# Performance work log

Hardware: AMD Instinct MI355X
Metric: run time of the kernel (lower is better)

Reference implementation:

```python
import jax, jax.numpy as jnp
import numpy as np

H, C = 3, 64  # heads, per-head channels
NEG_SLOPE = 0.2

def setup_inputs() -> dict:
    key = jax.random.key(0)
    ks = jax.random.split(key, 8)
    B, N, D, E = 2, 50000, 128, 800000
    h = jax.random.normal(ks[0], (B, N, D), dtype=jnp.float32)
    edge_index = jax.random.randint(ks[1], (2, E), 0, N, dtype=jnp.int64)
    s = 1.0 / np.sqrt(D)
    W = jax.random.normal(ks[2], (D, H * C), dtype=jnp.float32) * s
    a_src = jax.random.normal(ks[3], (H, C), dtype=jnp.float32) * (1.0 / np.sqrt(C))
    a_dst = jax.random.normal(ks[4], (H, C), dtype=jnp.float32) * (1.0 / np.sqrt(C))
    bias = jnp.zeros((H * C,), dtype=jnp.float32)
    Wo = jax.random.normal(ks[5], (H * C, 1), dtype=jnp.float32) * (1.0 / np.sqrt(H * C))
    bo = jnp.zeros((1,), dtype=jnp.float32)
    return {"h": h, "edge_index": edge_index, "W": W, "a_src": a_src,
            "a_dst": a_dst, "bias": bias, "Wo": Wo, "bo": bo}

def _gat_single(h_b, src, dst, N, W, a_src, a_dst, bias):
    # h_b: [N, D] -> x: [N, H, C]
    x = (h_b @ W).reshape(-1, H, C)
    alpha_s = jnp.einsum('nhc,hc->nh', x, a_src)  # [N, H]
    alpha_d = jnp.einsum('nhc,hc->nh', x, a_dst)  # [N, H]
    e = alpha_s[src] + alpha_d[dst]               # [E', H]
    e = jnp.where(e > 0, e, NEG_SLOPE * e)        # leaky_relu(0.2)
    # segment softmax over edges grouped by destination node
    emax = jax.ops.segment_max(e, dst, num_segments=N)          # [N, H]
    p = jnp.exp(e - emax[dst])
    denom = jax.ops.segment_sum(p, dst, num_segments=N)         # [N, H]
    att = p / (denom[dst] + 1e-16)                               # [E', H]
    out = jax.ops.segment_sum(att[:, :, None] * x[src], dst, num_segments=N)  # [N,H,C]
    return out.reshape(-1, H * C) + bias

def reference(h, edge_index, W, a_src, a_dst, bias, Wo, bo):
    B, N, D = h.shape
    # PyG GATConv default: add self loops
    loops = jnp.arange(N, dtype=edge_index.dtype)
    src = jnp.concatenate([edge_index[0], loops])
    dst = jnp.concatenate([edge_index[1], loops])
    gat = jax.vmap(lambda hb: _gat_single(hb, src, dst, N, W, a_src, a_dst, bias))(h)
    gat = jax.nn.elu(gat)            # [B, N, H*C]; dropout inactive (eval)
    logits = gat @ Wo + bo           # [B, N, 1]
    return logits
```

## Files before the change

kernel.cpp:

```cpp
#include <hip/hip_runtime.h>
#include <hip/hip_bf16.h>
#include <math.h>

typedef __hip_bfloat16 bf16;
typedef __attribute__((ext_vector_type(8))) short short8;
typedef __attribute__((ext_vector_type(4))) short short4v;
typedef __attribute__((ext_vector_type(4))) float f32x4;
typedef __attribute__((ext_vector_type(2))) float f32x2;

#define HC 192
#define DIN 128
#define NEG_SLOPE 0.2f
#define GN 8
#define CAP 56
#define GROWS 128

static inline int cdiv(int a, int b){ return (a + b - 1) / b; }

__device__ inline short f2bf(float f){
  __hip_bfloat16 b = __float2bfloat16(f);
  return __builtin_bit_cast(short, b);
}
__device__ inline float loadf(const void* p, size_t i, int fm){
  return fm ? __bfloat162float(((const bf16*)p)[i]) : ((const float*)p)[i];
}
__device__ inline int eload(const void* p, long long i, int em){
  return em ? (int)(((const long long*)p)[i]) : ((const int*)p)[i];
}

__device__ inline int detect_fm(const unsigned* __restrict__ hw){
  unsigned w = hw[threadIdx.x & 63];
  unsigned expo = (w >> 7) & 0xFF;
  unsigned long long m = __ballot(expo >= 100 && expo <= 135);
  return __popcll(m) > 32;
}
__device__ inline int detect_em(const unsigned* __restrict__ ew){
  unsigned long long m = __ballot(ew[2*(threadIdx.x & 63) + 1] != 0);
  return __popcll(m) < 32;
}

__global__ void k_zero(int* __restrict__ counts, int N){
  int idx = blockIdx.x * 256 + threadIdx.x;
  for (int i = idx; i < N; i += 96 * 256) counts[i] = 0;
}

__global__ __launch_bounds__(512) void k_fused(const void* __restrict__ h,
    const void* __restrict__ W, const void* __restrict__ a_src,
    const void* __restrict__ a_dst, bf16* __restrict__ x,
    float* __restrict__ asp, float* __restrict__ adp,
    const void* __restrict__ ei, int* __restrict__ counts,
    unsigned* __restrict__ srcs, int M, int N, int E, int NBG){
  __shared__ alignas(16) short ldsW[HC * 136];
  __shared__ alignas(16) float asfL[HC];
  __shared__ alignas(16) float adfL[HC];

  if ((int)blockIdx.x >= NBG){
    int em = detect_em((const unsigned*)ei);
    int idx = ((int)blockIdx.x - NBG) * 512 + (int)threadIdx.x;
    if (idx >= E + N) return;
    int s, d;
    if (idx < E){
      s = eload(ei, idx, em);
      d = eload(ei, (long long)E + idx, em);
    } else { s = d = idx - E; }
    if ((unsigned)d >= (unsigned)N) return;
    if ((unsigned)s >= (unsigned)N) s = 0;
    int slot = atomicAdd(&counts[d], 1);
    if (slot >= CAP) return;
    srcs[(size_t)d * CAP + slot] = (unsigned)s;
    return;
  }

  int fm   = detect_fm((const unsigned*)h);
  int tid  = threadIdx.x;
  int w    = tid >> 6;
  int lane = tid & 63;
  int r16  = lane & 15;
  int quad = lane >> 4;
  if (tid < HC)           asfL[tid]        = loadf(a_src, tid, fm);
  else if (tid < 2 * HC)  adfL[tid - HC]   = loadf(a_dst, tid - HC, fm);
  for (int pi = tid; pi < HC * 16; pi += 512){
    int j = pi % HC, dblk = pi / HC;
    short8 v8;
    #pragma unroll
    for (int kk = 0; kk < 8; kk++)
      v8[kk] = f2bf(loadf(W, (size_t)(dblk * 8 + kk) * HC + j, fm));
    *(short8*)&ldsW[j * 136 + dblk * 8] = v8;
  }
  __syncthreads();

  int row  = (int)blockIdx.x * GROWS + w * 16 + r16;
  int lrow = min(row, M - 1);
  f32x4 acc[12];
  #pragma unroll
  for (int i = 0; i < 12; i++) acc[i] = (f32x4){0.f,0.f,0.f,0.f};
  size_t hbase = (size_t)lrow * DIN + quad * 8;
  #pragma unroll
  for (int kb = 0; kb < 4; kb++){
    short8 bh;
    if (fm == 0){
      const float* hf = (const float*)h + hbase + kb * 32;
      float4 a = *(const float4*)hf;
      float4 b = *(const float4*)(hf + 4);
      bh[0]=f2bf(a.x); bh[1]=f2bf(a.y); bh[2]=f2bf(a.z); bh[3]=f2bf(a.w);
      bh[4]=f2bf(b.x); bh[5]=f2bf(b.y); bh[6]=f2bf(b.z); bh[7]=f2bf(b.w);
    } else {
      bh = *(const short8*)((const bf16*)h + hbase + kb * 32);
    }
    #pragma unroll
    for (int nt = 0; nt < 12; nt++){
      short8 aw = *(const short8*)&ldsW[(nt*16 + r16) * 136 + kb * 32 + quad * 8];
      acc[nt] = __builtin_amdgcn_mfma_f32_16x16x32_bf16(aw, bh, acc[nt], 0,0,0);
    }
  }
  if (row < M){
    int bb    = row >= N;
    int nodeR = row - bb * N;
    bf16* xr  = x + ((size_t)nodeR * 2 + bb) * HC;
    #pragma unroll
    for (int nt = 0; nt < 12; nt++){
      short4v pk = { f2bf(acc[nt][0]), f2bf(acc[nt][1]),
                     f2bf(acc[nt][2]), f2bf(acc[nt][3]) };
      *(short4v*)(xr + nt*16 + quad*4) = pk;
    }
  }
  float vs[3] = {0.f,0.f,0.f}, vd[3] = {0.f,0.f,0.f};
  #pragma unroll
  for (int nt = 0; nt < 12; nt++){
    int hh = nt >> 2;
    f32x4 a4 = *(const f32x4*)&asfL[nt*16 + quad*4];
    f32x4 d4 = *(const f32x4*)&adfL[nt*16 + quad*4];
    vs[hh] += acc[nt][0]*a4[0] + acc[nt][1]*a4[1] + acc[nt][2]*a4[2] + acc[nt][3]*a4[3];
    vd[hh] += acc[nt][0]*d4[0] + acc[nt][1]*d4[1] + acc[nt][2]*d4[2] + acc[nt][3]*d4[3];
  }
  #pragma unroll
  for (int hh = 0; hh < 3; hh++){
    float v1 = vs[hh], v2 = vd[hh];
    v1 += __shfl_down(v1, 32);  v1 += __shfl_down(v1, 16);
    v2 += __shfl_down(v2, 32);  v2 += __shfl_down(v2, 16);
    if (lane < 16 && row < M){
      int b = row >= N;
      int node = row - b * N;
      asp[(size_t)node*8 + b*3 + hh] = v1;
      adp[(size_t)node*8 + b*3 + hh] = v2;
    }
  }
}

__global__ __launch_bounds__(512) void k_gat(const bf16* __restrict__ x,
    const unsigned* __restrict__ srcs, const int* __restrict__ cnt,
    const float* __restrict__ asp, const float* __restrict__ adp,
    const void* __restrict__ bias, const void* __restrict__ Wo,
    const void* __restrict__ bo, const unsigned* __restrict__ hw,
    float* __restrict__ out, int N){
  int fm   = detect_fm(hw);
  int blk  = blockIdx.x;
  int t    = threadIdx.x;
  __shared__ int      csL[GN];
  __shared__ float    adl[GN * 6];
  __shared__ unsigned ldsS[GN * CAP];
  __shared__ float    ldsP[GN * CAP * 6];
  __shared__ alignas(16) float biasL[HC];
  __shared__ alignas(16) float WoL[HC];
  __shared__ float    boL;
  if (t < HC)           biasL[t]      = loadf(bias, t, fm);
  else if (t < 2 * HC)  WoL[t - HC]   = loadf(Wo, t - HC, fm);
  else if (t == 511)    boL           = loadf(bo, 0, fm);
  if (t < GN){
    int nd = GN*blk + t;
    csL[t] = (nd < N) ? min(cnt[nd], CAP) : 0;
  }
  if (t < GN * 6){
    int nd = t / 6, k = t - nd * 6;
    int nodeid = GN*blk + nd;
    adl[t] = (nodeid < N) ? adp[(size_t)nodeid * 8 + k] : 0.f;
  }
  __syncthreads();
  if (t < GN * CAP){
    int nd = t / CAP, sl = t - nd * CAP;
    if (sl < csL[nd]){
      int s = (int)srcs[(size_t)(GN*blk + nd) * CAP + sl];
      ldsS[t] = (unsigned)s;
      float4 A0 = *(const float4*)(asp + (size_t)s * 8);
      float4 A1 = *(const float4*)(asp + (size_t)s * 8 + 4);
      float e0 = A0.x + adl[nd*6+0], e1 = A0.y + adl[nd*6+1];
      float e2 = A0.z + adl[nd*6+2], e3 = A0.w + adl[nd*6+3];
      float e4 = A1.x + adl[nd*6+4], e5 = A1.y + adl[nd*6+5];
      e0 = e0 > 0.f ? e0 : NEG_SLOPE*e0;  e1 = e1 > 0.f ? e1 : NEG_SLOPE*e1;
      e2 = e2 > 0.f ? e2 : NEG_SLOPE*e2;  e3 = e3 > 0.f ? e3 : NEG_SLOPE*e3;
      e4 = e4 > 0.f ? e4 : NEG_SLOPE*e4;  e5 = e5 > 0.f ? e5 : NEG_SLOPE*e5;
      ldsP[t*6 + 0] = __expf(e0);  ldsP[t*6 + 1] = __expf(e1);
      ldsP[t*6 + 2] = __expf(e2);  ldsP[t*6 + 3] = __expf(e3);
      ldsP[t*6 + 4] = __expf(e4);  ldsP[t*6 + 5] = __expf(e5);
    }
  }
  __syncthreads();

  int w    = t >> 6;
  int lane = t & 63;
  int node = GN*blk + w;
  float r  = 0.f;
  if (node < N){
    int b     = lane & 1;
    int c8    = lane >> 1;
    int mycnt = csL[w];
    int rbase = w * CAP;
    if (c8 < 24){
      int hh   = c8 >> 3;
      int pidx = b*3 + hh;
      const ushort* xb = (const ushort*)x + b * HC + c8 * 8;
      f32x2 a0 = {0.f,0.f}, a1 = {0.f,0.f}, a2 = {0.f,0.f}, a3 = {0.f,0.f};
      float den = 0.f;
      auto LD = [&](int i) -> uint4 {
        int s = (int)ldsS[rbase + i];
        return *(const uint4*)(xb + (size_t)s * (2 * HC));
      };
      auto PROC = [&](int i, uint4 q){
        float p = ldsP[(rbase + i)*6 + pidx];
        den += p;
        f32x2 pp = {p, p};
        f32x2 v;
        v[0] = __uint_as_float(q.x << 16); v[1] = __uint_as_float(q.x & 0xffff0000u);
        a0 += pp * v;
        v[0] = __uint_as_float(q.y << 16); v[1] = __uint_as_float(q.y & 0xffff0000u);
        a1 += pp * v;
        v[0] = __uint_as_float(q.z << 16); v[1] = __uint_as_float(q.z & 0xffff0000u);
        a2 += pp * v;
        v[0] = __uint_as_float(q.w << 16); v[1] = __uint_as_float(q.w & 0xffff0000u);
        a3 += pp * v;
      };
      uint4 q0 = {}, q1 = {}, q2 = {};
      if (mycnt > 0) q0 = LD(0);
      if (mycnt > 1) q1 = LD(1);
      if (mycnt > 2) q2 = LD(2);
      int i = 0;
      for (; i + 3 <= mycnt; i += 3){
        PROC(i,     q0); if (i + 3 < mycnt) q0 = LD(i + 3);
        PROC(i + 1, q1); if (i + 4 < mycnt) q1 = LD(i + 4);
        PROC(i + 2, q2); if (i + 5 < mycnt) q2 = LD(i + 5);
      }
      if (i     < mycnt) PROC(i,     q0);
      if (i + 1 < mycnt) PROC(i + 1, q1);
      float inv = 1.f / (den + 1e-16f);
      f32x4 bi0 = *(const f32x4*)&biasL[c8*8];
      f32x4 bi1 = *(const f32x4*)&biasL[c8*8 + 4];
      f32x4 w0  = *(const f32x4*)&WoL[c8*8];
      f32x4 w1  = *(const f32x4*)&WoL[c8*8 + 4];
      float v;
      v = a0[0]*inv + bi0[0]; v = v > 0.f ? v : expm1f(v); r += v * w0[0];
      v = a0[1]*inv + bi0[1]; v = v > 0.f ? v : expm1f(v); r += v * w0[1];
      v = a1[0]*inv + bi0[2]; v = v > 0.f ? v : expm1f(v); r += v * w0[2];
      v = a1[1]*inv + bi0[3]; v = v > 0.f ? v : expm1f(v); r += v * w0[3];
      v = a2[0]*inv + bi1[0]; v = v > 0.f ? v : expm1f(v); r += v * w1[0];
      v = a2[1]*inv + bi1[1]; v = v > 0.f ? v : expm1f(v); r += v * w1[1];
      v = a3[0]*inv + bi1[2]; v = v > 0.f ? v : expm1f(v); r += v * w1[2];
      v = a3[1]*inv + bi1[3]; v = v > 0.f ? v : expm1f(v); r += v * w1[3];
    }
  }
  r += __shfl_xor(r, 2);
  r += __shfl_xor(r, 4);
  r += __shfl_xor(r, 8);
  r += __shfl_xor(r, 16);
  r += __shfl_xor(r, 32);
  if (lane < 2 && node < N)
    out[(size_t)lane * N + node] = r + boL;
}

extern "C" void kernel_launch(void* const* d_in, const int* in_sizes, int n_in,
                              void* d_out, int out_size, void* d_ws, size_t ws_size,
                              hipStream_t stream){
  const void* h     = d_in[0];
  const void* ei    = d_in[1];
  const void* W     = d_in[2];
  const void* a_src = d_in[3];
  const void* a_dst = d_in[4];
  const void* bias  = d_in[5];
  const void* Wo    = d_in[6];
  const void* bo    = d_in[7];
  float* out = (float*)d_out;

  const int M    = in_sizes[0] / DIN;
  const int N    = M / 2;
  const int E    = in_sizes[1] / 2;
  const int Etot = E + N;

  char* ws = (char*)d_ws;
  size_t off = 0;
  auto alloc = [&](size_t bytes) -> void* {
    void* p = ws + off;
    off = (off + bytes + 511) & ~(size_t)511;
    return p;
  };
  bf16*     x      = (bf16*)    alloc((size_t)M * HC * sizeof(bf16));
  float*    asp    = (float*)   alloc((size_t)N * 8 * sizeof(float));
  float*    adp    = (float*)   alloc((size_t)N * 8 * sizeof(float));
  int*      counts = (int*)     alloc((size_t)N * sizeof(int));
  unsigned* srcs   = (unsigned*)alloc((size_t)N * CAP * sizeof(unsigned));
  (void)ws_size; (void)n_in; (void)out_size;

  const int NBG = cdiv(M, GROWS);
  const int NBB = cdiv(Etot, 512);

  k_zero<<<96, 256, 0, stream>>>(counts, N);
  k_fused<<<NBG + NBB, 512, 0, stream>>>(h, W, a_src, a_dst, x, asp, adp,
      ei, counts, srcs, M, N, E, NBG);
  k_gat<<<cdiv(N, GN), 512, 0, stream>>>(x, srcs, counts, asp, adp,
      bias, Wo, bo, (const unsigned*)h, out, N);
}
```

Baseline: 266.2 us.

## Merge three launches into one persistent cooperative kernel with grid syncs

Replaces the zero, GEMM+bucket, and GAT aggregation launches with a single persistent cooperative kernel. It uses grid-wide syncs between phases and a union of shared-memory layouts, with grid-stride loops over tiles and groups. The edge gather loop is also reworked to batch 8 or 4 independent row loads before accumulating. This aims to remove launch gaps, but it caps occupancy at the cooperative grid size, adds grid barrier cost, and loses overlap between the GEMM and bucketing blocks. The original launches are kept as a fallback.

```diff
diff --git a/kernel.cpp b/kernel.cpp
--- a/kernel.cpp
+++ b/kernel.cpp
@@ -1,6 +1,9 @@
 #include <hip/hip_runtime.h>
 #include <hip/hip_bf16.h>
+#include <hip/hip_cooperative_groups.h>
 #include <math.h>
+
+namespace cg = cooperative_groups;
 
 typedef __hip_bfloat16 bf16;
 typedef __attribute__((ext_vector_type(8))) short short8;
@@ -39,57 +42,46 @@
   return __popcll(m) < 32;
 }
 
-__global__ void k_zero(int* __restrict__ counts, int N){
-  int idx = blockIdx.x * 256 + threadIdx.x;
-  for (int i = idx; i < N; i += 96 * 256) counts[i] = 0;
-}
-
-__global__ __launch_bounds__(512) void k_fused(const void* __restrict__ h,
-    const void* __restrict__ W, const void* __restrict__ a_src,
-    const void* __restrict__ a_dst, bf16* __restrict__ x,
-    float* __restrict__ asp, float* __restrict__ adp,
-    const void* __restrict__ ei, int* __restrict__ counts,
-    unsigned* __restrict__ srcs, int M, int N, int E, int NBG){
-  __shared__ alignas(16) short ldsW[HC * 136];
-  __shared__ alignas(16) float asfL[HC];
-  __shared__ alignas(16) float adfL[HC];
-
-  if ((int)blockIdx.x >= NBG){
-    int em = detect_em((const unsigned*)ei);
-    int idx = ((int)blockIdx.x - NBG) * 512 + (int)threadIdx.x;
-    if (idx >= E + N) return;
-    int s, d;
-    if (idx < E){
-      s = eload(ei, idx, em);
-      d = eload(ei, (long long)E + idx, em);
-    } else { s = d = idx - E; }
-    if ((unsigned)d >= (unsigned)N) return;
-    if ((unsigned)s >= (unsigned)N) s = 0;
-    int slot = atomicAdd(&counts[d], 1);
-    if (slot >= CAP) return;
-    srcs[(size_t)d * CAP + slot] = (unsigned)s;
-    return;
-  }
-
-  int fm   = detect_fm((const unsigned*)h);
+struct GemmLds {
+  alignas(16) short ldsW[HC * 136];
+  alignas(16) float asfL[HC];
+  alignas(16) float adfL[HC];
+};
+struct GatLds {
+  int      csL[GN];
+  float    adl[GN * 6];
+  alignas(16) unsigned ldsS[GN * CAP];
+  alignas(16) float    ldsP[GN * CAP * 6];
+  alignas(16) float    biasL[HC];
+  alignas(16) float    WoL[HC];
+  float    boL;
+};
+union AllLds { GemmLds g; GatLds a; };
+
+__device__ __forceinline__ void dev_stage_gemm(GemmLds& L, const void* W,
+    const void* a_src, const void* a_dst, int fm){
+  int tid = threadIdx.x;
+  if (tid < HC)          L.asfL[tid]      = loadf(a_src, tid, fm);
+  else if (tid < 2*HC)   L.adfL[tid-HC]   = loadf(a_dst, tid-HC, fm);
+  for (int pi = tid; pi < HC * 16; pi += 512){
+    int j = pi % HC, dblk = pi / HC;
+    short8 v8;
+    #pragma unroll
+    for (int kk = 0; kk < 8; kk++)
+      v8[kk] = f2bf(loadf(W, (size_t)(dblk*8 + kk) * HC + j, fm));
+    *(short8*)&L.ldsW[j * 136 + dblk * 8] = v8;
+  }
+}
+
+__device__ __forceinline__ void dev_gemm_tile(GemmLds& L, int tile,
+    const void* __restrict__ h, bf16* __restrict__ x,
+    float* __restrict__ asp, float* __restrict__ adp, int M, int N, int fm){
   int tid  = threadIdx.x;
   int w    = tid >> 6;
   int lane = tid & 63;
   int r16  = lane & 15;
   int quad = lane >> 4;
-  if (tid < HC)           asfL[tid]        = loadf(a_src, tid, fm);
-  else if (tid < 2 * HC)  adfL[tid - HC]   = loadf(a_dst, tid - HC, fm);
-  for (int pi = tid; pi < HC * 16; pi += 512){
-    int j = pi % HC, dblk = pi / HC;
-    short8 v8;
-    #pragma unroll
-    for (int kk = 0; kk < 8; kk++)
-      v8[kk] = f2bf(loadf(W, (size_t)(dblk * 8 + kk) * HC + j, fm));
-    *(short8*)&ldsW[j * 136 + dblk * 8] = v8;
-  }
-  __syncthreads();
-
-  int row  = (int)blockIdx.x * GROWS + w * 16 + r16;
+  int row  = tile * GROWS + w * 16 + r16;
   int lrow = min(row, M - 1);
   f32x4 acc[12];
   #pragma unroll
@@ -109,7 +101,7 @@
     }
     #pragma unroll
     for (int nt = 0; nt < 12; nt++){
-      short8 aw = *(const short8*)&ldsW[(nt*16 + r16) * 136 + kb * 32 + quad * 8];
+      short8 aw = *(const short8*)&L.ldsW[(nt*16 + r16) * 136 + kb * 32 + quad * 8];
       acc[nt] = __builtin_amdgcn_mfma_f32_16x16x32_bf16(aw, bh, acc[nt], 0,0,0);
     }
   }
@@ -128,8 +120,8 @@
   #pragma unroll
   for (int nt = 0; nt < 12; nt++){
     int hh = nt >> 2;
-    f32x4 a4 = *(const f32x4*)&asfL[nt*16 + quad*4];
-    f32x4 d4 = *(const f32x4*)&adfL[nt*16 + quad*4];
+    f32x4 a4 = *(const f32x4*)&L.asfL[nt*16 + quad*4];
+    f32x4 d4 = *(const f32x4*)&L.adfL[nt*16 + quad*4];
     vs[hh] += acc[nt][0]*a4[0] + acc[nt][1]*a4[1] + acc[nt][2]*a4[2] + acc[nt][3]*a4[3];
     vd[hh] += acc[nt][0]*d4[0] + acc[nt][1]*d4[1] + acc[nt][2]*d4[2] + acc[nt][3]*d4[3];
   }
@@ -147,105 +139,112 @@
   }
 }
 
-__global__ __launch_bounds__(512) void k_gat(const bf16* __restrict__ x,
-    const unsigned* __restrict__ srcs, const int* __restrict__ cnt,
-    const float* __restrict__ asp, const float* __restrict__ adp,
-    const void* __restrict__ bias, const void* __restrict__ Wo,
-    const void* __restrict__ bo, const unsigned* __restrict__ hw,
-    float* __restrict__ out, int N){
-  int fm   = detect_fm(hw);
-  int blk  = blockIdx.x;
-  int t    = threadIdx.x;
-  __shared__ int      csL[GN];
-  __shared__ float    adl[GN * 6];
-  __shared__ unsigned ldsS[GN * CAP];
-  __shared__ float    ldsP[GN * CAP * 6];
-  __shared__ alignas(16) float biasL[HC];
-  __shared__ alignas(16) float WoL[HC];
-  __shared__ float    boL;
-  if (t < HC)           biasL[t]      = loadf(bias, t, fm);
-  else if (t < 2 * HC)  WoL[t - HC]   = loadf(Wo, t - HC, fm);
-  else if (t == 511)    boL           = loadf(bo, 0, fm);
+__device__ __forceinline__ void dev_bucket(int idx, const void* __restrict__ ei,
+    int em, int E, int N, int* __restrict__ counts, unsigned* __restrict__ srcs){
+  if (idx >= E + N) return;
+  int s, d;
+  if (idx < E){
+    s = eload(ei, idx, em);
+    d = eload(ei, (long long)E + idx, em);
+  } else { s = d = idx - E; }
+  if ((unsigned)d >= (unsigned)N) return;
+  if ((unsigned)s >= (unsigned)N) s = 0;
+  int slot = atomicAdd(&counts[d], 1);
+  if (slot >= CAP) return;
+  srcs[(size_t)d * CAP + slot] = (unsigned)s;
+}
+
+#define GPROC(QQ, RI) do{                                                     \
+    float p = L.ldsP[(RI)*6 + pidx];                                          \
+    den += p;                                                                 \
+    f32x2 pp = {p, p}; f32x2 v;                                               \
+    v[0]=__uint_as_float((QQ).x<<16); v[1]=__uint_as_float((QQ).x&0xffff0000u); a0+=pp*v; \
+    v[0]=__uint_as_float((QQ).y<<16); v[1]=__uint_as_float((QQ).y&0xffff0000u); a1+=pp*v; \
+    v[0]=__uint_as_float((QQ).z<<16); v[1]=__uint_as_float((QQ).z&0xffff0000u); a2+=pp*v; \
+    v[0]=__uint_as_float((QQ).w<<16); v[1]=__uint_as_float((QQ).w&0xffff0000u); a3+=pp*v; \
+  }while(0)
+
+__device__ __forceinline__ void dev_gat_group(GatLds& L, int grp,
+    const bf16* __restrict__ x, const unsigned* __restrict__ srcs,
+    const int* __restrict__ cnt, const float* __restrict__ asp,
+    const float* __restrict__ adp, float* __restrict__ out, int N){
+  int t = threadIdx.x;
   if (t < GN){
-    int nd = GN*blk + t;
-    csL[t] = (nd < N) ? min(cnt[nd], CAP) : 0;
+    int nd = GN*grp + t;
+    L.csL[t] = (nd < N) ? min(cnt[nd], CAP) : 0;
   }
   if (t < GN * 6){
     int nd = t / 6, k = t - nd * 6;
-    int nodeid = GN*blk + nd;
-    adl[t] = (nodeid < N) ? adp[(size_t)nodeid * 8 + k] : 0.f;
+    int nodeid = GN*grp + nd;
+    L.adl[t] = (nodeid < N) ? adp[(size_t)nodeid * 8 + k] : 0.f;
   }
   __syncthreads();
   if (t < GN * CAP){
     int nd = t / CAP, sl = t - nd * CAP;
-    if (sl < csL[nd]){
-      int s = (int)srcs[(size_t)(GN*blk + nd) * CAP + sl];
-      ldsS[t] = (unsigned)s;
+    if (sl < L.csL[nd]){
+      int s = (int)srcs[(size_t)(GN*grp + nd) * CAP + sl];
+      L.ldsS[t] = (unsigned)s;
       float4 A0 = *(const float4*)(asp + (size_t)s * 8);
       float4 A1 = *(const float4*)(asp + (size_t)s * 8 + 4);
-      float e0 = A0.x + adl[nd*6+0], e1 = A0.y + adl[nd*6+1];
-      float e2 = A0.z + adl[nd*6+2], e3 = A0.w + adl[nd*6+3];
-      float e4 = A1.x + adl[nd*6+4], e5 = A1.y + adl[nd*6+5];
+      float e0 = A0.x + L.adl[nd*6+0], e1 = A0.y + L.adl[nd*6+1];
+      float e2 = A0.z + L.adl[nd*6+2], e3 = A0.w + L.adl[nd*6+3];
+      float e4 = A1.x + L.adl[nd*6+4], e5 = A1.y + L.adl[nd*6+5];
       e0 = e0 > 0.f ? e0 : NEG_SLOPE*e0;  e1 = e1 > 0.f ? e1 : NEG_SLOPE*e1;
       e2 = e2 > 0.f ? e2 : NEG_SLOPE*e2;  e3 = e3 > 0.f ? e3 : NEG_SLOPE*e3;
       e4 = e4 > 0.f ? e4 : NEG_SLOPE*e4;  e5 = e5 > 0.f ? e5 : NEG_SLOPE*e5;
-      ldsP[t*6 + 0] = __expf(e0);  ldsP[t*6 + 1] = __expf(e1);
-      ldsP[t*6 + 2] = __expf(e2);  ldsP[t*6 + 3] = __expf(e3);
-      ldsP[t*6 + 4] = __expf(e4);  ldsP[t*6 + 5] = __expf(e5);
+      L.ldsP[t*6 + 0] = __expf(e0);  L.ldsP[t*6 + 1] = __expf(e1);
+      L.ldsP[t*6 + 2] = __expf(e2);  L.ldsP[t*6 + 3] = __expf(e3);
+      L.ldsP[t*6 + 4] = __expf(e4);  L.ldsP[t*6 + 5] = __expf(e5);
     }
   }
   __syncthreads();
 
   int w    = t >> 6;
   int lane = t & 63;
-  int node = GN*blk + w;
+  int node = GN*grp + w;
   float r  = 0.f;
   if (node < N){
     int b     = lane & 1;
     int c8    = lane >> 1;
-    int mycnt = csL[w];
+    int mycnt = L.csL[w];
     int rbase = w * CAP;
     if (c8 < 24){
-      int hh   = c8 >> 3;
-      int pidx = b*3 + hh;
+      int pidx = b*3 + (c8 >> 3);
       const ushort* xb = (const ushort*)x + b * HC + c8 * 8;
       f32x2 a0 = {0.f,0.f}, a1 = {0.f,0.f}, a2 = {0.f,0.f}, a3 = {0.f,0.f};
       float den = 0.f;
-      auto LD = [&](int i) -> uint4 {
-        int s = (int)ldsS[rbase + i];
-        return *(const uint4*)(xb + (size_t)s * (2 * HC));
-      };
-      auto PROC = [&](int i, uint4 q){
-        float p = ldsP[(rbase + i)*6 + pidx];
-        den += p;
-        f32x2 pp = {p, p};
-        f32x2 v;
-        v[0] = __uint_as_float(q.x << 16); v[1] = __uint_as_float(q.x & 0xffff0000u);
-        a0 += pp * v;
-        v[0] = __uint_as_float(q.y << 16); v[1] = __uint_as_float(q.y & 0xffff0000u);
-        a1 += pp * v;
-        v[0] = __uint_as_float(q.z << 16); v[1] = __uint_as_float(q.z & 0xffff0000u);
-        a2 += pp * v;
-        v[0] = __uint_as_float(q.w << 16); v[1] = __uint_as_float(q.w & 0xffff0000u);
-        a3 += pp * v;
-      };
-      uint4 q0 = {}, q1 = {}, q2 = {};
-      if (mycnt > 0) q0 = LD(0);
-      if (mycnt > 1) q1 = LD(1);
-      if (mycnt > 2) q2 = LD(2);
       int i = 0;
-      for (; i + 3 <= mycnt; i += 3){
-        PROC(i,     q0); if (i + 3 < mycnt) q0 = LD(i + 3);
-        PROC(i + 1, q1); if (i + 4 < mycnt) q1 = LD(i + 4);
-        PROC(i + 2, q2); if (i + 5 < mycnt) q2 = LD(i + 5);
+      for (; i + 8 <= mycnt; i += 8){
+        uint4 q[8];
+        #pragma unroll
+        for (int k = 0; k < 8; k++){
+          int s = (int)L.ldsS[rbase + i + k];
+          q[k] = *(const uint4*)(xb + (size_t)s * (2 * HC));
+        }
+        #pragma unroll
+        for (int k = 0; k < 8; k++) GPROC(q[k], rbase + i + k);
       }
-      if (i     < mycnt) PROC(i,     q0);
-      if (i + 1 < mycnt) PROC(i + 1, q1);
+      if (i + 4 <= mycnt){
+        uint4 q[4];
+        #pragma unroll
+        for (int k = 0; k < 4; k++){
+          int s = (int)L.ldsS[rbase + i + k];
+          q[k] = *(const uint4*)(xb + (size_t)s * (2 * HC));
+        }
+        #pragma unroll
+        for (int k = 0; k < 4; k++) GPROC(q[k], rbase + i + k);
+        i += 4;
+      }
+      for (; i < mycnt; i++){
+        int s = (int)L.ldsS[rbase + i];
+        uint4 q = *(const uint4*)(xb + (size_t)s * (2 * HC));
+        GPROC(q, rbase + i);
+      }
       float inv = 1.f / (den + 1e-16f);
-      f32x4 bi0 = *(const f32x4*)&biasL[c8*8];
-      f32x4 bi1 = *(const f32x4*)&biasL[c8*8 + 4];
-      f32x4 w0  = *(const f32x4*)&WoL[c8*8];
-      f32x4 w1  = *(const f32x4*)&WoL[c8*8 + 4];
+      f32x4 bi0 = *(const f32x4*)&L.biasL[c8*8];
+      f32x4 bi1 = *(const f32x4*)&L.biasL[c8*8 + 4];
+      f32x4 w0  = *(const f32x4*)&L.WoL[c8*8];
+      f32x4 w1  = *(const f32x4*)&L.WoL[c8*8 + 4];
       float v;
       v = a0[0]*inv + bi0[0]; v = v > 0.f ? v : expm1f(v); r += v * w0[0];
       v = a0[1]*inv + bi0[1]; v = v > 0.f ? v : expm1f(v); r += v * w0[1];
@@ -263,7 +262,72 @@
   r += __shfl_xor(r, 16);
   r += __shfl_xor(r, 32);
   if (lane < 2 && node < N)
-    out[(size_t)lane * N + node] = r + boL;
+    out[(size_t)lane * N + node] = r + L.boL;
+  __syncthreads();
+}
+
+__global__ __launch_bounds__(512) void k_all(const void* h, const void* W,
+    const void* a_src, const void* a_dst, const void* bias, const void* Wo,
+    const void* bo, const void* ei, bf16* x, float* asp, float* adp,
+    int* counts, unsigned* srcs, float* out, int M, int N, int E,
+    int NBG, int NBB, int NGAT){
+  cg::grid_group grid = cg::this_grid();
+  __shared__ AllLds U;
+  int bid = blockIdx.x, t = threadIdx.x;
+  int nb  = gridDim.x;
+  int fm  = detect_fm((const unsigned*)h);
+  for (int i = bid * 512 + t; i < N; i += nb * 512) counts[i] = 0;
+  __threadfence();
+  grid.sync();
+  __threadfence();
+  dev_stage_gemm(U.g, W, a_src, a_dst, fm);
+  __syncthreads();
+  for (int tile = bid; tile < NBG; tile += nb)
+    dev_gemm_tile(U.g, tile, h, x, asp, adp, M, N, fm);
+  {
+    int em = detect_em((const unsigned*)ei);
+    for (int ch = bid; ch < NBB; ch += nb)
+      dev_bucket(ch * 512 + t, ei, em, E, N, counts, srcs);
+  }
+  __threadfence();
+  grid.sync();
+  __threadfence();
+  if (t < HC)          U.a.biasL[t]    = loadf(bias, t, fm);
+  else if (t < 2*HC)   U.a.WoL[t-HC]   = loadf(Wo, t-HC, fm);
+  else if (t == 511)   U.a.boL         = loadf(bo, 0, fm);
+  for (int grp = bid; grp < NGAT; grp += nb)
+    dev_gat_group(U.a, grp, x, srcs, counts, asp, adp, out, N);
+}
+
+__global__ void k_zero(int* __restrict__ counts, int N){
+  int idx = blockIdx.x * 256 + threadIdx.x;
+  for (int i = idx; i < N; i += 96 * 256) counts[i] = 0;
+}
+__global__ __launch_bounds__(512) void k_fused_fb(const void* h, const void* W,
+    const void* a_src, const void* a_dst, bf16* x, float* asp, float* adp,
+    const void* ei, int* counts, unsigned* srcs, int M, int N, int E, int NBG){
+  __shared__ GemmLds L;
+  if ((int)blockIdx.x >= NBG){
+    int em = detect_em((const unsigned*)ei);
+    dev_bucket(((int)blockIdx.x - NBG) * 512 + (int)threadIdx.x,
+               ei, em, E, N, counts, srcs);
+    return;
+  }
+  int fm = detect_fm((const unsigned*)h);
+  dev_stage_gemm(L, W, a_src, a_dst, fm);
+  __syncthreads();
+  dev_gemm_tile(L, blockIdx.x, h, x, asp, adp, M, N, fm);
+}
+__global__ __launch_bounds__(512) void k_gat_fb(const bf16* x, const unsigned* srcs,
+    const int* cnt, const float* asp, const float* adp, const void* bias,
+    const void* Wo, const void* bo, const unsigned* hw, float* out, int N){
+  __shared__ GatLds L;
+  int fm = detect_fm(hw);
+  int t  = threadIdx.x;
+  if (t < HC)          L.biasL[t]    = loadf(bias, t, fm);
+  else if (t < 2*HC)   L.WoL[t-HC]   = loadf(Wo, t-HC, fm);
+  else if (t == 511)   L.boL         = loadf(bo, 0, fm);
+  dev_gat_group(L, blockIdx.x, x, srcs, cnt, asp, adp, out, N);
 }
 
 extern "C" void kernel_launch(void* const* d_in, const int* in_sizes, int n_in,
@@ -298,12 +362,41 @@
   unsigned* srcs   = (unsigned*)alloc((size_t)N * CAP * sizeof(unsigned));
   (void)ws_size; (void)n_in; (void)out_size;
 
-  const int NBG = cdiv(M, GROWS);
-  const int NBB = cdiv(Etot, 512);
-
-  k_zero<<<96, 256, 0, stream>>>(counts, N);
-  k_fused<<<NBG + NBB, 512, 0, stream>>>(h, W, a_src, a_dst, x, asp, adp,
-      ei, counts, srcs, M, N, E, NBG);
-  k_gat<<<cdiv(N, GN), 512, 0, stream>>>(x, srcs, counts, asp, adp,
-      bias, Wo, bo, (const unsigned*)h, out, N);
-}
+  const int NBG  = cdiv(M, GROWS);
+  const int NBB  = cdiv(Etot, 512);
+  const int NGAT = cdiv(N, GN);
+
+  static int g_grid = -2;
+  if (g_grid == -2){
+    int coop = 0, dev = 0, bpm = 0;
+    hipGetDevice(&dev);
+    hipDeviceGetAttribute(&coop, hipDeviceAttributeCooperativeLaunch, dev);
+    if (coop){
+      hipError_t e = hipOccupancyMaxActiveBlocksPerMultiprocessor(&bpm, k_all, 512, 0);
+      if (e != hipSuccess) bpm = 0;
+    }
+    g_grid = (coop && bpm > 0) ? bpm * 256 : 0;
+    if (g_grid > 768) g_grid = 768;
+  }
+
+  bool done = false;
+  if (g_grid > 0){
+    int MM = M, NN = N, EE = E, nbg = NBG, nbb = NBB, ngat = NGAT;
+    void* args[] = {(void*)&h, (void*)&W, (void*)&a_src, (void*)&a_dst,
+                    (void*)&bias, (void*)&Wo, (void*)&bo, (void*)&ei,
+                    (void*)&x, (void*)&asp, (void*)&adp, (void*)&counts,
+                    (void*)&srcs, (void*)&out, (void*)&MM, (void*)&NN,
+                    (void*)&EE, (void*)&nbg, (void*)&nbb, (void*)&ngat};
+    hipError_t e = hipLaunchCooperativeKernel(k_all, dim3(g_grid), dim3(512),
+                                              args, 0, stream);
+    done = (e == hipSuccess);
+    if (!done) g_grid = 0;
+  }
+  if (!done){
+    k_zero<<<96, 256, 0, stream>>>(counts, N);
+    k_fused_fb<<<NBG + NBB, 512, 0, stream>>>(h, W, a_src, a_dst, x, asp, adp,
+        ei, counts, srcs, M, N, E, NBG);
+    k_gat_fb<<<NGAT, 512, 0, stream>>>(x, srcs, counts, asp, adp,
+        bias, Wo, bo, (const unsigned*)h, out, N);
+  }
+}
```

Measured after the change: 274.2 us. 1.03x slower.

## Dynamically schedule GAT nodes per block with fp16 attention weights and batched gathers

Applied to the files above, without the earlier changes.

The aggregation kernel now handles 32 destination nodes per block. Each wave claims the next node through a shared atomic counter instead of owning exactly one node, which balances uneven in-degrees across waves. Attention weights are stored as packed fp16 in LDS to halve shared-memory use, and neighbour rows are gathered eight at a time behind a scheduling barrier to raise memory-level parallelism. Padding slots are zero-filled so the loop can round up to multiples of eight, at the cost of extra wasted gathers of row 0 and reduced precision in the attention weights. The GEMM kernel is only refactored into helper functions.

```diff
diff --git a/kernel.cpp b/kernel.cpp
--- a/kernel.cpp
+++ b/kernel.cpp
@@ -11,7 +11,7 @@
 #define HC 192
 #define DIN 128
 #define NEG_SLOPE 0.2f
-#define GN 8
+#define GN 32
 #define CAP 56
 #define GROWS 128
 
@@ -26,6 +26,15 @@
 }
 __device__ inline int eload(const void* p, long long i, int em){
   return em ? (int)(((const long long*)p)[i]) : ((const int*)p)[i];
+}
+__device__ inline unsigned pack2h(float a, float b){
+  unsigned short ha = __builtin_bit_cast(unsigned short, (_Float16)a);
+  unsigned short hb = __builtin_bit_cast(unsigned short, (_Float16)b);
+  return (unsigned)ha | ((unsigned)hb << 16);
+}
+__device__ inline float unph(unsigned w, int hi){
+  unsigned short hs = hi ? (unsigned short)(w >> 16) : (unsigned short)(w & 0xffff);
+  return (float)__builtin_bit_cast(_Float16, hs);
 }
 
 __device__ inline int detect_fm(const unsigned* __restrict__ hw){
@@ -44,52 +53,36 @@
   for (int i = idx; i < N; i += 96 * 256) counts[i] = 0;
 }
 
-__global__ __launch_bounds__(512) void k_fused(const void* __restrict__ h,
-    const void* __restrict__ W, const void* __restrict__ a_src,
-    const void* __restrict__ a_dst, bf16* __restrict__ x,
-    float* __restrict__ asp, float* __restrict__ adp,
-    const void* __restrict__ ei, int* __restrict__ counts,
-    unsigned* __restrict__ srcs, int M, int N, int E, int NBG){
-  __shared__ alignas(16) short ldsW[HC * 136];
-  __shared__ alignas(16) float asfL[HC];
-  __shared__ alignas(16) float adfL[HC];
-
-  if ((int)blockIdx.x >= NBG){
-    int em = detect_em((const unsigned*)ei);
-    int idx = ((int)blockIdx.x - NBG) * 512 + (int)threadIdx.x;
-    if (idx >= E + N) return;
-    int s, d;
-    if (idx < E){
-      s = eload(ei, idx, em);
-      d = eload(ei, (long long)E + idx, em);
-    } else { s = d = idx - E; }
-    if ((unsigned)d >= (unsigned)N) return;
-    if ((unsigned)s >= (unsigned)N) s = 0;
-    int slot = atomicAdd(&counts[d], 1);
-    if (slot >= CAP) return;
-    srcs[(size_t)d * CAP + slot] = (unsigned)s;
-    return;
-  }
-
-  int fm   = detect_fm((const unsigned*)h);
+struct GemmLds {
+  alignas(16) short ldsW[HC * 136];
+  alignas(16) float asfL[HC];
+  alignas(16) float adfL[HC];
+};
+
+__device__ __forceinline__ void dev_stage_gemm(GemmLds& L, const void* W,
+    const void* a_src, const void* a_dst, int fm){
+  int tid = threadIdx.x;
+  if (tid < HC)          L.asfL[tid]      = loadf(a_src, tid, fm);
+  else if (tid < 2*HC)   L.adfL[tid-HC]   = loadf(a_dst, tid-HC, fm);
+  for (int pi = tid; pi < HC * 16; pi += 512){
+    int j = pi % HC, dblk = pi / HC;
+    short8 v8;
+    #pragma unroll
+    for (int kk = 0; kk < 8; kk++)
+      v8[kk] = f2bf(loadf(W, (size_t)(dblk*8 + kk) * HC + j, fm));
+    *(short8*)&L.ldsW[j * 136 + dblk * 8] = v8;
+  }
+}
+
+__device__ __forceinline__ void dev_gemm_tile(GemmLds& L, int tile,
+    const void* __restrict__ h, bf16* __restrict__ x,
+    float* __restrict__ asp, float* __restrict__ adp, int M, int N, int fm){
   int tid  = threadIdx.x;
   int w    = tid >> 6;
   int lane = tid & 63;
   int r16  = lane & 15;
   int quad = lane >> 4;
-  if (tid < HC)           asfL[tid]        = loadf(a_src, tid, fm);
-  else if (tid < 2 * HC)  adfL[tid - HC]   = loadf(a_dst, tid - HC, fm);
-  for (int pi = tid; pi < HC * 16; pi += 512){
-    int j = pi % HC, dblk = pi / HC;
-    short8 v8;
-    #pragma unroll
-    for (int kk = 0; kk < 8; kk++)
-      v8[kk] = f2bf(loadf(W, (size_t)(dblk * 8 + kk) * HC + j, fm));
-    *(short8*)&ldsW[j * 136 + dblk * 8] = v8;
-  }
-  __syncthreads();
-
-  int row  = (int)blockIdx.x * GROWS + w * 16 + r16;
+  int row  = tile * GROWS + w * 16 + r16;
   int lrow = min(row, M - 1);
   f32x4 acc[12];
   #pragma unroll
@@ -109,7 +102,7 @@
     }
     #pragma unroll
     for (int nt = 0; nt < 12; nt++){
-      short8 aw = *(const short8*)&ldsW[(nt*16 + r16) * 136 + kb * 32 + quad * 8];
+      short8 aw = *(const short8*)&L.ldsW[(nt*16 + r16) * 136 + kb * 32 + quad * 8];
       acc[nt] = __builtin_amdgcn_mfma_f32_16x16x32_bf16(aw, bh, acc[nt], 0,0,0);
     }
   }
@@ -128,8 +121,8 @@
   #pragma unroll
   for (int nt = 0; nt < 12; nt++){
     int hh = nt >> 2;
-    f32x4 a4 = *(const f32x4*)&asfL[nt*16 + quad*4];
-    f32x4 d4 = *(const f32x4*)&adfL[nt*16 + quad*4];
+    f32x4 a4 = *(const f32x4*)&L.asfL[nt*16 + quad*4];
+    f32x4 d4 = *(const f32x4*)&L.adfL[nt*16 + quad*4];
     vs[hh] += acc[nt][0]*a4[0] + acc[nt][1]*a4[1] + acc[nt][2]*a4[2] + acc[nt][3]*a4[3];
     vd[hh] += acc[nt][0]*d4[0] + acc[nt][1]*d4[1] + acc[nt][2]*d4[2] + acc[nt][3]*d4[3];
   }
@@ -147,40 +140,74 @@
   }
 }
 
-__global__ __launch_bounds__(512) void k_gat(const bf16* __restrict__ x,
+__device__ __forceinline__ void dev_bucket(int idx, const void* __restrict__ ei,
+    int em, int E, int N, int* __restrict__ counts, unsigned* __restrict__ srcs){
+  if (idx >= E + N) return;
+  int s, d;
+  if (idx < E){
+    s = eload(ei, idx, em);
+    d = eload(ei, (long long)E + idx, em);
+  } else { s = d = idx - E; }
+  if ((unsigned)d >= (unsigned)N) return;
+  if ((unsigned)s >= (unsigned)N) s = 0;
+  int slot = atomicAdd(&counts[d], 1);
+  if (slot >= CAP) return;
+  srcs[(size_t)d * CAP + slot] = (unsigned)s;
+}
+
+__global__ __launch_bounds__(512) void k_fused(const void* h, const void* W,
+    const void* a_src, const void* a_dst, bf16* x, float* asp, float* adp,
+    const void* ei, int* counts, unsigned* srcs, int M, int N, int E, int NBG){
+  __shared__ GemmLds L;
+  if ((int)blockIdx.x >= NBG){
+    int em = detect_em((const unsigned*)ei);
+    dev_bucket(((int)blockIdx.x - NBG) * 512 + (int)threadIdx.x,
+               ei, em, E, N, counts, srcs);
+    return;
+  }
+  int fm = detect_fm((const unsigned*)h);
+  dev_stage_gemm(L, W, a_src, a_dst, fm);
+  __syncthreads();
+  dev_gemm_tile(L, blockIdx.x, h, x, asp, adp, M, N, fm);
+}
+
+__global__ __launch_bounds__(512, 8) void k_gat(const bf16* __restrict__ x,
     const unsigned* __restrict__ srcs, const int* __restrict__ cnt,
     const float* __restrict__ asp, const float* __restrict__ adp,
     const void* __restrict__ bias, const void* __restrict__ Wo,
     const void* __restrict__ bo, const unsigned* __restrict__ hw,
     float* __restrict__ out, int N){
-  int fm   = detect_fm(hw);
-  int blk  = blockIdx.x;
-  int t    = threadIdx.x;
+  int fm  = detect_fm(hw);
+  int blk = blockIdx.x;
+  int t   = threadIdx.x;
   __shared__ int      csL[GN];
+  __shared__ int      nextn;
   __shared__ float    adl[GN * 6];
   __shared__ unsigned ldsS[GN * CAP];
-  __shared__ float    ldsP[GN * CAP * 6];
+  __shared__ unsigned ldsPh[GN * CAP * 3];
   __shared__ alignas(16) float biasL[HC];
   __shared__ alignas(16) float WoL[HC];
-  __shared__ float    boL;
-  if (t < HC)           biasL[t]      = loadf(bias, t, fm);
-  else if (t < 2 * HC)  WoL[t - HC]   = loadf(Wo, t - HC, fm);
-  else if (t == 511)    boL           = loadf(bo, 0, fm);
+  __shared__ float boL;
+  if (t < HC)          biasL[t]    = loadf(bias, t, fm);
+  else if (t < 2*HC)   WoL[t-HC]   = loadf(Wo, t-HC, fm);
+  else if (t == 511)   boL         = loadf(bo, 0, fm);
   if (t < GN){
     int nd = GN*blk + t;
     csL[t] = (nd < N) ? min(cnt[nd], CAP) : 0;
   }
-  if (t < GN * 6){
-    int nd = t / 6, k = t - nd * 6;
+  if (t == GN) nextn = 8;
+  if (t >= 64 && t < 64 + GN * 6){
+    int j = t - 64;
+    int nd = j / 6, k = j - nd * 6;
     int nodeid = GN*blk + nd;
-    adl[t] = (nodeid < N) ? adp[(size_t)nodeid * 8 + k] : 0.f;
+    adl[j] = (nodeid < N) ? adp[(size_t)nodeid * 8 + k] : 0.f;
   }
   __syncthreads();
-  if (t < GN * CAP){
-    int nd = t / CAP, sl = t - nd * CAP;
+  for (int j = t; j < GN * CAP; j += 512){
+    int nd = j / CAP, sl = j - nd * CAP;
     if (sl < csL[nd]){
       int s = (int)srcs[(size_t)(GN*blk + nd) * CAP + sl];
-      ldsS[t] = (unsigned)s;
+      ldsS[j] = (unsigned)s;
       float4 A0 = *(const float4*)(asp + (size_t)s * 8);
       float4 A1 = *(const float4*)(asp + (size_t)s * 8 + 4);
       float e0 = A0.x + adl[nd*6+0], e1 = A0.y + adl[nd*6+1];
@@ -189,81 +216,89 @@
       e0 = e0 > 0.f ? e0 : NEG_SLOPE*e0;  e1 = e1 > 0.f ? e1 : NEG_SLOPE*e1;
       e2 = e2 > 0.f ? e2 : NEG_SLOPE*e2;  e3 = e3 > 0.f ? e3 : NEG_SLOPE*e3;
       e4 = e4 > 0.f ? e4 : NEG_SLOPE*e4;  e5 = e5 > 0.f ? e5 : NEG_SLOPE*e5;
-      ldsP[t*6 + 0] = __expf(e0);  ldsP[t*6 + 1] = __expf(e1);
-      ldsP[t*6 + 2] = __expf(e2);  ldsP[t*6 + 3] = __expf(e3);
-      ldsP[t*6 + 4] = __expf(e4);  ldsP[t*6 + 5] = __expf(e5);
+      ldsPh[j*3 + 0] = pack2h(__expf(e0), __expf(e1));
+      ldsPh[j*3 + 1] = pack2h(__expf(e2), __expf(e3));
+      ldsPh[j*3 + 2] = pack2h(__expf(e4), __expf(e5));
+    } else {
+      ldsS[j] = 0u;
+      ldsPh[j*3 + 0] = 0u;  ldsPh[j*3 + 1] = 0u;  ldsPh[j*3 + 2] = 0u;
     }
   }
   __syncthreads();
 
   int w    = t >> 6;
   int lane = t & 63;
-  int node = GN*blk + w;
-  float r  = 0.f;
-  if (node < N){
-    int b     = lane & 1;
-    int c8    = lane >> 1;
-    int mycnt = csL[w];
-    int rbase = w * CAP;
-    if (c8 < 24){
-      int hh   = c8 >> 3;
-      int pidx = b*3 + hh;
-      const ushort* xb = (const ushort*)x + b * HC + c8 * 8;
-      f32x2 a0 = {0.f,0.f}, a1 = {0.f,0.f}, a2 = {0.f,0.f}, a3 = {0.f,0.f};
-      float den = 0.f;
-      auto LD = [&](int i) -> uint4 {
-        int s = (int)ldsS[rbase + i];
-        return *(const uint4*)(xb + (size_t)s * (2 * HC));
-      };
-      auto PROC = [&](int i, uint4 q){
-        float p = ldsP[(rbase + i)*6 + pidx];
-        den += p;
-        f32x2 pp = {p, p};
-        f32x2 v;
-        v[0] = __uint_as_float(q.x << 16); v[1] = __uint_as_float(q.x & 0xffff0000u);
-        a0 += pp * v;
-        v[0] = __uint_as_float(q.y << 16); v[1] = __uint_as_float(q.y & 0xffff0000u);
-        a1 += pp * v;
-        v[0] = __uint_as_float(q.z << 16); v[1] = __uint_as_float(q.z & 0xffff0000u);
-        a2 += pp * v;
-        v[0] = __uint_as_float(q.w << 16); v[1] = __uint_as_float(q.w & 0xffff0000u);
-        a3 += pp * v;
-      };
-      uint4 q0 = {}, q1 = {}, q2 = {};
-      if (mycnt > 0) q0 = LD(0);
-      if (mycnt > 1) q1 = LD(1);
-      if (mycnt > 2) q2 = LD(2);
-      int i = 0;
-      for (; i + 3 <= mycnt; i += 3){
-        PROC(i,     q0); if (i + 3 < mycnt) q0 = LD(i + 3);
-        PROC(i + 1, q1); if (i + 4 < mycnt) q1 = LD(i + 4);
-        PROC(i + 2, q2); if (i + 5 < mycnt) q2 = LD(i + 5);
-      }
-      if (i     < mycnt) PROC(i,     q0);
-      if (i + 1 < mycnt) PROC(i + 1, q1);
+  int b    = lane & 1;
+  int c8   = lane >> 1;
+  bool act = c8 < 24;
+  int pidx = b*3 + (c8 >> 3);
+  int pwi  = pidx >> 1, pwh = pidx & 1;
+  unsigned myoff = act ? (unsigned)(b*384 + c8*16) : 0u;
+  const char* xB0 = (const char*)x;
+
+  int mynode = w;
+  while (mynode < GN){
+    int nd    = GN*blk + mynode;
+    int cntn  = csL[mynode];
+    int nit   = (cntn + 7) & ~7;
+    int rbase = mynode * CAP;
+    f32x2 a0 = {0.f,0.f}, a1 = {0.f,0.f}, a2 = {0.f,0.f}, a3 = {0.f,0.f};
+    float den = 0.f;
+
+#define LDQ(K, RI) { unsigned s = ldsS[RI]; \
+    q##K = *(const uint4*)(xB0 + (size_t)(s * 768u + myoff)); }
+#define GPROC(QQ, RI) do{ \
+    float p = unph(ldsPh[(RI)*3 + pwi], pwh); \
+    den += p; \
+    f32x2 pp = {p, p}; f32x2 v; \
+    v[0]=__uint_as_float((QQ).x<<16); v[1]=__uint_as_float((QQ).x&0xffff0000u); a0+=pp*v; \
+    v[0]=__uint_as_float((QQ).y<<16); v[1]=__uint_as_float((QQ).y&0xffff0000u); a1+=pp*v; \
+    v[0]=__uint_as_float((QQ).z<<16); v[1]=__uint_as_float((QQ).z&0xffff0000u); a2+=pp*v; \
+    v[0]=__uint_as_float((QQ).w<<16); v[1]=__uint_as_float((QQ).w&0xffff0000u); a3+=pp*v; \
+  }while(0)
+
+    for (int i = 0; i < nit; i += 8){
+      int rb = rbase + i;
+      uint4 q0, q1, q2, q3, q4, q5, q6, q7;
+      LDQ(0, rb+0); LDQ(1, rb+1); LDQ(2, rb+2); LDQ(3, rb+3);
+      LDQ(4, rb+4); LDQ(5, rb+5); LDQ(6, rb+6); LDQ(7, rb+7);
+      __builtin_amdgcn_sched_barrier(0);
+      GPROC(q0, rb+0); GPROC(q1, rb+1); GPROC(q2, rb+2); GPROC(q3, rb+3);
+      GPROC(q4, rb+4); GPROC(q5, rb+5); GPROC(q6, rb+6); GPROC(q7, rb+7);
+    }
+#undef LDQ
+#undef GPROC
+
+    float r = 0.f;
+    if (act && nd < N){
       float inv = 1.f / (den + 1e-16f);
       f32x4 bi0 = *(const f32x4*)&biasL[c8*8];
       f32x4 bi1 = *(const f32x4*)&biasL[c8*8 + 4];
       f32x4 w0  = *(const f32x4*)&WoL[c8*8];
       f32x4 w1  = *(const f32x4*)&WoL[c8*8 + 4];
       float v;
-      v = a0[0]*inv + bi0[0]; v = v > 0.f ? v : expm1f(v); r += v * w0[0];
-      v = a0[1]*inv + bi0[1]; v = v > 0.f ? v : expm1f(v); r += v * w0[1];
-      v = a1[0]*inv + bi0[2]; v = v > 0.f ? v : expm1f(v); r += v * w0[2];
-      v = a1[1]*inv + bi0[3]; v = v > 0.f ? v : expm1f(v); r += v * w0[3];
-      v = a2[0]*inv + bi1[0]; v = v > 0.f ? v : expm1f(v); r += v * w1[0];
-      v = a2[1]*inv + bi1[1]; v = v > 0.f ? v : expm1f(v); r += v * w1[1];
-      v = a3[0]*inv + bi1[2]; v = v > 0.f ? v : expm1f(v); r += v * w1[2];
-      v = a3[1]*inv + bi1[3]; v = v > 0.f ? v : expm1f(v); r += v * w1[3];
-    }
-  }
-  r += __shfl_xor(r, 2);
-  r += __shfl_xor(r, 4);
-  r += __shfl_xor(r, 8);
-  r += __shfl_xor(r, 16);
-  r += __shfl_xor(r, 32);
-  if (lane < 2 && node < N)
-    out[(size_t)lane * N + node] = r + boL;
+      v = a0[0]*inv + bi0[0]; v = v > 0.f ? v : __expf(v)-1.f; r += v * w0[0];
+      v = a0[1]*inv + bi0[1]; v = v > 0.f ? v : __expf(v)-1.f; r += v * w0[1];
+      v = a1[0]*inv + bi0[2]; v = v > 0.f ? v : __expf(v)-1.f; r += v * w0[2];
+      v = a1[1]*inv + bi0[3]; v = v > 0.f ? v : __expf(v)-1.f; r += v * w0[3];
+      v = a2[0]*inv + bi1[0]; v = v > 0.f ? v : __expf(v)-1.f; r += v * w1[0];
+      v = a2[1]*inv + bi1[1]; v = v > 0.f ? v : __expf(v)-1.f; r += v * w1[1];
+      v = a3[0]*inv + bi1[2]; v = v > 0.f ? v : __expf(v)-1.f; r += v * w1[2];
+      v = a3[1]*inv + bi1[3]; v = v > 0.f ? v : __expf(v)-1.f; r += v * w1[3];
+    }
+    r += __shfl_xor(r, 2);
+    r += __shfl_xor(r, 4);
+    r += __shfl_xor(r, 8);
+    r += __shfl_xor(r, 16);
+    r += __shfl_xor(r, 32);
+    if (lane < 2 && nd < N)
+      out[(size_t)lane * N + nd] = r + boL;
+
+    int nx;
+    if (lane == 0) nx = atomicAdd(&nextn, 1);
+    nx = __shfl(nx, 0);
+    mynode = nx;
+  }
 }
 
 extern "C" void kernel_launch(void* const* d_in, const int* in_sizes, int n_in,
@@ -298,12 +333,13 @@
   unsigned* srcs   = (unsigned*)alloc((size_t)N * CAP * sizeof(unsigned));
   (void)ws_size; (void)n_in; (void)out_size;
 
-  const int NBG = cdiv(M, GROWS);
-  const int NBB = cdiv(Etot, 512);
+  const int NBG  = cdiv(M, GROWS);
+  const int NBB  = cdiv(Etot, 512);
+  const int NGAT = cdiv(N, GN);
 
   k_zero<<<96, 256, 0, stream>>>(counts, N);
   k_fused<<<NBG + NBB, 512, 0, stream>>>(h, W, a_src, a_dst, x, asp, adp,
       ei, counts, srcs, M, N, E, NBG);
-  k_gat<<<cdiv(N, GN), 512, 0, stream>>>(x, srcs, counts, asp, adp,
+  k_gat<<<NGAT, 512, 0, stream>>>(x, srcs, counts, asp, adp,
       bias, Wo, bo, (const unsigned*)h, out, N);
 }
```

Result: slower. 275.3 us (+3.4%).
